# Optimization experiments

Hardware: AMD Instinct MI355X
Metric: run time of the kernel (lower is better)

## Reference

```python
import jax, jax.numpy as jnp
import numpy as np

ALPHA_MGD = 2e-05
NOISE_SIGMA = 8.0
NOISE_VAR = NOISE_SIGMA ** 2  # 64.0


def _conv2d(x, w, b, pad):
    # x: [N,C,H,W], w: [O,I,kh,kw]
    y = jax.lax.conv_general_dilated(
        x, w, window_strides=(1, 1), padding=[(pad, pad), (pad, pad)],
        dimension_numbers=("NCHW", "OIHW", "NCHW"))
    return y + b[None, :, None, None]


def setup_inputs() -> dict:
    key = jax.random.key(0)
    ks = jax.random.split(key, 8)
    N, Cs, Ct, H, W = 8, 128, 256, 64, 64
    return {
        "preds_S": jax.random.normal(ks[0], (N, Cs, H, W), jnp.float32),
        "preds_T": jax.random.normal(ks[1], (N, Ct, H, W), jnp.float32),
        "W_align": jax.random.normal(ks[2], (Ct, Cs, 1, 1), jnp.float32) * 0.05,
        "b_align": jnp.zeros((Ct,), jnp.float32),
        "W_gen1": jax.random.normal(ks[3], (Ct, Ct, 3, 3), jnp.float32) * 0.02,
        "b_gen1": jnp.zeros((Ct,), jnp.float32),
        "W_gen2": jax.random.normal(ks[4], (Ct, Ct, 3, 3), jnp.float32) * 0.02,
        "b_gen2": jnp.zeros((Ct,), jnp.float32),
    }


def reference(preds_S, preds_T, W_align, b_align, W_gen1, b_gen1, W_gen2, b_gen2):
    # align student channels to teacher channels (1x1 conv)
    s = _conv2d(preds_S, W_align, b_align, pad=0)
    N, C, H, W = preds_T.shape
    # deterministic checkerboard mask: tile([[0,1],[1,0]]) cropped to HxW -> (h+w) % 2
    hh = jnp.arange(H)[:, None]
    ww = jnp.arange(W)[None, :]
    mat = ((hh + ww) % 2).astype(s.dtype)  # [H,W]
    masked_fea = s * mat  # broadcast over [N,C,H,W]
    # generation network: conv3x3 -> relu -> conv3x3
    new_fea = _conv2d(jax.nn.relu(_conv2d(masked_fea, W_gen1, b_gen1, pad=1)), W_gen2, b_gen2, pad=1)
    # bmc_loss_md(pred=preds_T, target=new_fea, noise_var=64):
    # logits[i,j] = MVN(pred_i, noise_var*I).log_prob(target_j); the normalization
    # constant is class-independent and cancels in cross-entropy, keep the quadratic term.
    p = preds_T.reshape(N, -1)   # [N, D], D = C*H*W
    t = new_fea.reshape(N, -1)   # [N, D]
    # pairwise squared L2 via ||p||^2 + ||t||^2 - 2 p.t  (avoids NxNxD blow-up)
    sq = (jnp.sum(p * p, axis=1)[:, None]
          + jnp.sum(t * t, axis=1)[None, :]
          - 2.0 * (p @ t.T))  # [N, N]
    logits = -0.5 * sq / NOISE_VAR
    # cross_entropy(logits, arange(N)) = mean_i (logsumexp_j logits[i,j] - logits[i,i])
    ce = jnp.mean(jax.nn.logsumexp(logits, axis=1) - jnp.diagonal(logits))
    loss = ce * (2.0 * NOISE_VAR) / N
    return loss * ALPHA_MGD
```

## Files before the change

kernel.cpp:

```cpp
#include <hip/hip_runtime.h>

typedef unsigned short u16;
typedef short short8 __attribute__((ext_vector_type(8)));
typedef unsigned short ushort8 __attribute__((ext_vector_type(8)));
typedef float floatx16 __attribute__((ext_vector_type(16)));

#define PLANE8C  17952
#define NSTRIDEC 574464
#define PLANE8   34848
#define NSTRIDE  1115136

__device__ __forceinline__ u16 f2b(float f) {
  unsigned u = __builtin_bit_cast(unsigned, f);
  return (u16)((u + 0x7FFFu + ((u >> 16) & 1u)) >> 16);
}
__device__ __forceinline__ float b2f(u16 b) {
  return __builtin_bit_cast(float, ((unsigned)b) << 16);
}

typedef const __attribute__((address_space(1))) unsigned int* gptr_t;
typedef __attribute__((address_space(3))) unsigned int* sptr_t;

__global__ __launch_bounds__(256) void kprep(
    const float* __restrict__ Wg1, u16* __restrict__ Wsw1,
    const float* __restrict__ Wg2, u16* __restrict__ Wsw2,
    const float* __restrict__ Wa,  u16* __restrict__ Wb,
    const float* __restrict__ pS,  u16* __restrict__ T,
    u16* __restrict__ maskedC, u16* __restrict__ t1)
{
  __shared__ u16 Ls[64 * 136];
  int b = blockIdx.x, t = threadIdx.x;

  if (b < 576) {
    const float* W = (b < 288) ? Wg1 : Wg2;
    u16* D = (b < 288) ? Wsw1 : Wsw2;
    int bb = (b < 288) ? b : b - 288;
    int cid = bb * 256 + t;
    int d = cid % 1152, ctcg = cid / 1152;
    int ct = ctcg & 3, cg = ctcg >> 2;
    int colow = d & 31, cihalf = (d >> 5) & 1, sc = (d >> 6) & 1, tap = d >> 7;
    int co = ct * 64 + sc * 32 + colow;
    short8 v;
    #pragma unroll
    for (int jj = 0; jj < 8; ++jj) {
      int ci = cg * 16 + cihalf * 8 + jj;
      v[jj] = (short)f2b(W[((size_t)(co * 256 + ci)) * 9 + tap]);
    }
    *(short8*)&D[(size_t)cid * 8] = v;
  } else if (b < 592) {
    int v = (b - 576) * 256 + t;
    int colow = v & 31, hfb = (v >> 5) & 1, cog = (v >> 6) & 7, k = v >> 9;
    int co = cog * 32 + colow;
    int ci0 = k * 16 + hfb * 8;
    float4 f0 = *(const float4*)(Wa + (size_t)co * 128 + ci0);
    float4 f1 = *(const float4*)(Wa + (size_t)co * 128 + ci0 + 4);
    short8 o;
    o[0] = (short)f2b(f0.x); o[1] = (short)f2b(f0.y);
    o[2] = (short)f2b(f0.z); o[3] = (short)f2b(f0.w);
    o[4] = (short)f2b(f1.x); o[5] = (short)f2b(f1.y);
    o[6] = (short)f2b(f1.z); o[7] = (short)f2b(f1.w);
    *(short8*)&Wb[(size_t)v * 8] = o;
  } else if (b < 1104) {
    int bb = b - 592;
    int n = bb >> 6, pt = bb & 63, pix0 = pt * 64;
    int ci = t >> 1, ph = t & 1;
    const float* src = pS + ((size_t)n * 128 + ci) * 4096 + pix0 + ph * 32;
    #pragma unroll
    for (int i = 0; i < 8; ++i) {
      float4 v4 = *(const float4*)(src + i * 4);
      int pix = ph * 32 + i * 4;
      Ls[(pix + 0) * 136 + ci] = f2b(v4.x);
      Ls[(pix + 1) * 136 + ci] = f2b(v4.y);
      Ls[(pix + 2) * 136 + ci] = f2b(v4.z);
      Ls[(pix + 3) * 136 + ci] = f2b(v4.w);
    }
    __syncthreads();
    int p = t >> 2, q = t & 3;
    const u16* row = Ls + p * 136 + q * 32;
    u16* dst = T + ((size_t)n * 4096 + pix0 + p) * 128 + q * 32;
    #pragma unroll
    for (int k2 = 0; k2 < 4; ++k2)
      *(ushort8*)(dst + k2 * 8) = *(const ushort8*)(row + k2 * 8);
  } else if (b < 1360) {
    int p = b - 1104;
    u16* base = maskedC + (size_t)(p >> 5) * NSTRIDEC + (size_t)(p & 31) * PLANE8C;
    short8 z;
    #pragma unroll
    for (int jj = 0; jj < 8; ++jj) z[jj] = 0;
    if (t < 200) {
      int off;
      if (t < 34)       off = t * 8;
      else if (t < 68)  off = (65 * 34 + (t - 34)) * 8;
      else if (t < 134) off = ((t - 68) * 34) * 8;
      else              off = ((t - 134) * 34 + 33) * 8;
      *(short8*)(base + off) = z;
    }
  } else {
    int p = b - 1360;
    u16* base = t1 + (size_t)(p >> 5) * NSTRIDE + (size_t)(p & 31) * PLANE8;
    short8 z;
    #pragma unroll
    for (int jj = 0; jj < 8; ++jj) z[jj] = 0;
    #pragma unroll
    for (int pass = 0; pass < 2; ++pass) {
      int seg = t + pass * 256;
      if (seg < 264) {
        int off;
        if (seg < 66)       off = seg * 8;
        else if (seg < 132) off = (65 * 66 + (seg - 66)) * 8;
        else if (seg < 198) off = ((seg - 132) * 66) * 8;
        else                off = ((seg - 198) * 66 + 65) * 8;
        *(short8*)(base + off) = z;
      }
    }
  }
}

__global__ __launch_bounds__(256) void k1m(const u16* __restrict__ T,
    const u16* __restrict__ Wb, const float* __restrict__ ba,
    u16* __restrict__ mk)
{
  __shared__ __align__(16) u16 Wl[32768];
  int b = blockIdx.x;
  int n = b >> 5, pt = b & 31;
  int t = threadIdx.x, wid = t >> 6, lane = t & 63;
  int ml = lane & 31, hf = lane >> 5;

  #pragma unroll
  for (int kk = 0; kk < 16; ++kk) {
    int chunk = kk * 256 + t;
    __builtin_amdgcn_global_load_lds((gptr_t)(const void*)(Wb + (size_t)chunk * 8),
                                     (sptr_t)(void*)(Wl + chunk * 8), 16, 0, 0);
  }

  const u16* Tn = T + (size_t)n * 524288;
  const u16* ap[4];
  #pragma unroll
  for (int g = 0; g < 4; ++g)
    ap[g] = Tn + (size_t)(pt * 128 + g * 32 + ml) * 128 + hf * 8;

  floatx16 acc[2][4];
  #pragma unroll
  for (int q = 0; q < 2; ++q)
    #pragma unroll
    for (int g = 0; g < 4; ++g)
      #pragma unroll
      for (int i = 0; i < 16; ++i) acc[q][g][i] = 0.f;

  __syncthreads();

  const short8* WlV = (const short8*)Wl;
  int cogb = wid * 2;

  short8 a0[4], a1[4];
  #pragma unroll
  for (int g = 0; g < 4; ++g) a0[g] = *(const short8*)(ap[g]);

#define K1M_STEP(K, CUR, NXT, LAST)                                           \
  {                                                                           \
    if (!(LAST)) {                                                            \
      _Pragma("unroll")                                                       \
      for (int g = 0; g < 4; ++g)                                             \
        NXT[g] = *(const short8*)(ap[g] + ((K) + 1) * 16);                    \
    }                                                                         \
    short8 w0 = WlV[((K) * 8 + cogb) * 64 + lane];                            \
    short8 w1 = WlV[((K) * 8 + cogb + 1) * 64 + lane];                        \
    _Pragma("unroll")                                                         \
    for (int g = 0; g < 4; ++g) {                                             \
      acc[0][g] = __builtin_amdgcn_mfma_f32_32x32x16_bf16(CUR[g], w0, acc[0][g], 0, 0, 0); \
      acc[1][g] = __builtin_amdgcn_mfma_f32_32x32x16_bf16(CUR[g], w1, acc[1][g], 0, 0, 0); \
    }                                                                         \
  }
  K1M_STEP(0, a0, a1, 0)
  K1M_STEP(1, a1, a0, 0)
  K1M_STEP(2, a0, a1, 0)
  K1M_STEP(3, a1, a0, 0)
  K1M_STEP(4, a0, a1, 0)
  K1M_STEP(5, a1, a0, 0)
  K1M_STEP(6, a0, a1, 0)
  K1M_STEP(7, a1, a0, 1)
#undef K1M_STEP

  int co0 = cogb * 32 + ml, co1 = co0 + 32;
  float b0 = ba[co0], b1 = ba[co1];
  u16* base0 = mk + (size_t)n * NSTRIDEC + (size_t)(co0 >> 3) * PLANE8C + (co0 & 7);
  u16* base1 = mk + (size_t)n * NSTRIDEC + (size_t)(co1 >> 3) * PLANE8C + (co1 & 7);
  #pragma unroll
  for (int g = 0; g < 4; ++g)
    #pragma unroll
    for (int reg = 0; reg < 16; ++reg) {
      int m = (reg & 3) + 8 * (reg >> 2) + 4 * hf;
      int pix = pt * 128 + g * 32 + m;
      int h = pix >> 6, w = pix & 63;
      if (((h + w) & 1) == 1) {
        int j = (w - ((h + 1) & 1)) >> 1;
        int off = ((h + 1) * 34 + 1 + j) * 8;
        base0[off] = f2b(acc[0][g][reg] + b0);
        base1[off] = f2b(acc[1][g][reg] + b1);
      }
    }
}

__global__ __launch_bounds__(512) void kconvs(
    const u16* __restrict__ IN, const u16* __restrict__ WS,
    const float* __restrict__ bg, u16* __restrict__ OUT)
{
  __shared__ __align__(16) u16 L[30720];
  u16* LinA = L;
  u16* LwA  = L + 6144;
  u16* LinB = L + 15360;
  u16* LwB  = L + 21504;

  int b = blockIdx.x;
  int rt = b & 7, ct = (b >> 3) & 3, n = b >> 5;
  int h0 = rt * 8;
  int t = threadIdx.x;
  int wid = t >> 6, lane = t & 63;
  int hf = lane >> 5, ml = lane & 31;
  int e = wid & 1;

  const u16* inb = IN + (size_t)n * NSTRIDEC;
  const u16* wg  = WS + (size_t)ct * 1152 * 8;

  floatx16 acc[2][2];
  #pragma unroll
  for (int p = 0; p < 2; ++p)
    #pragma unroll
    for (int q = 0; q < 2; ++q)
      #pragma unroll
      for (int i = 0; i < 16; ++i) acc[p][q][i] = 0.f;

  auto STAGE = [&](int cg, u16* LinD, u16* LwD) {
    #pragma unroll
    for (int k = 0; k < 4; ++k) {
      int seg = wid + 8 * k;
      if (seg < 18) {
        const u16* src = wg + (size_t)cg * 36864 + (size_t)(seg * 64 + lane) * 8;
        __builtin_amdgcn_global_load_lds((gptr_t)(const void*)src,
                                         (sptr_t)(void*)(LwD + seg * 512), 16, 0, 0);
      } else if (seg < 30) {
        int ii = seg - 18;
        int hh = ii >= 6 ? 1 : 0;
        int s = ii - hh * 6;
        const u16* src = inb + (size_t)cg * (2 * PLANE8C) + (size_t)hh * PLANE8C
                         + (size_t)(h0 * 34 + s * 64 + lane) * 8;
        __builtin_amdgcn_global_load_lds((gptr_t)(const void*)src,
                                         (sptr_t)(void*)(LinD + (hh * 384 + s * 64) * 8),
                                         16, 0, 0);
      }
    }
  };

  auto COMPUTE = [&](const u16* LinS, const u16* LwS) {
    const short8* LinV = (const short8*)LinS;
    const short8* LwV  = (const short8*)LwS;
    int rA = hf * 384 + wid * 34 + 1 + ml;
    int rS = rA + 34;
    int rB = rA + 68;
    short8 iA0 = LinV[rA];
    short8 iS0 = LinV[rS];
    short8 iB0 = LinV[rB];
    short8 iSm = LinV[rS + e - 1];
    short8 iSp = LinV[rS + e];
    short8 iAm = LinV[rA - e];
    short8 iAp = LinV[rA + 1 - e];
    short8 iBm = LinV[rB - e];
    short8 iBp = LinV[rB + 1 - e];
    #pragma unroll
    for (int q = 0; q < 2; ++q) {
      short8 w0 = LwV[0 * 128 + q * 64 + lane];
      short8 w1 = LwV[1 * 128 + q * 64 + lane];
      short8 w2 = LwV[2 * 128 + q * 64 + lane];
      short8 w3 = LwV[3 * 128 + q * 64 + lane];
      short8 w4 = LwV[4 * 128 + q * 64 + lane];
      short8 w5 = LwV[5 * 128 + q * 64 + lane];
      short8 w6 = LwV[6 * 128 + q * 64 + lane];
      short8 w7 = LwV[7 * 128 + q * 64 + lane];
      short8 w8 = LwV[8 * 128 + q * 64 + lane];
      acc[0][q] = __builtin_amdgcn_mfma_f32_32x32x16_bf16(iA0, w1, acc[0][q], 0, 0, 0);
      acc[0][q] = __builtin_amdgcn_mfma_f32_32x32x16_bf16(iSm, w3, acc[0][q], 0, 0, 0);
      acc[0][q] = __builtin_amdgcn_mfma_f32_32x32x16_bf16(iSp, w5, acc[0][q], 0, 0, 0);
      acc[0][q] = __builtin_amdgcn_mfma_f32_32x32x16_bf16(iB0, w7, acc[0][q], 0, 0, 0);
      acc[1][q] = __builtin_amdgcn_mfma_f32_32x32x16_bf16(iAm, w0, acc[1][q], 0, 0, 0);
      acc[1][q] = __builtin_amdgcn_mfma_f32_32x32x16_bf16(iAp, w2, acc[1][q], 0, 0, 0);
      acc[1][q] = __builtin_amdgcn_mfma_f32_32x32x16_bf16(iS0, w4, acc[1][q], 0, 0, 0);
      acc[1][q] = __builtin_amdgcn_mfma_f32_32x32x16_bf16(iBm, w6, acc[1][q], 0, 0, 0);
      acc[1][q] = __builtin_amdgcn_mfma_f32_32x32x16_bf16(iBp, w8, acc[1][q], 0, 0, 0);
    }
  };

  STAGE(0, LinA, LwA);
  __syncthreads();
  for (int cg = 0; cg < 16; cg += 2) {
    STAGE(cg + 1, LinB, LwB);
    COMPUTE(LinA, LwA);
    __syncthreads();
    if (cg + 2 < 16) STAGE(cg + 2, LinA, LwA);
    COMPUTE(LinB, LwB);
    __syncthreads();
  }

  float bias0 = bg[ct * 64 + ml];
  float bias1 = bg[ct * 64 + 32 + ml];

  u16* ob = OUT + (size_t)n * NSTRIDE;
  int co0 = ct * 64 + ml, co1 = co0 + 32;
  int cb0 = ((co0 >> 4) * 2 + ((co0 >> 3) & 1)) * PLANE8 + (co0 & 7);
  int cb1 = ((co1 >> 4) * 2 + ((co1 >> 3) & 1)) * PLANE8 + (co1 & 7);
  int rowoff = (h0 + wid + 1) * 66 + 1;
  #pragma unroll
  for (int reg = 0; reg < 16; ++reg) {
    int m = (reg & 3) + 8 * (reg >> 2) + 4 * hf;
    int we = 2 * m + e, wo = 2 * m + 1 - e;
    float v;
    v = acc[0][0][reg] + bias0; v = fmaxf(v, 0.f); ob[cb0 + (rowoff + we) * 8] = f2b(v);
    v = acc[0][1][reg] + bias1; v = fmaxf(v, 0.f); ob[cb1 + (rowoff + we) * 8] = f2b(v);
    v = acc[1][0][reg] + bias0; v = fmaxf(v, 0.f); ob[cb0 + (rowoff + wo) * 8] = f2b(v);
    v = acc[1][1][reg] + bias1; v = fmaxf(v, 0.f); ob[cb1 + (rowoff + wo) * 8] = f2b(v);
  }
}

template <int MODE>
__global__ __launch_bounds__(512) void kconv(
    const u16* __restrict__ IN, const u16* __restrict__ WS,
    const float* __restrict__ bg, u16* __restrict__ OUT)
{
  __shared__ __align__(16) u16 L[40960];
  u16* LinA = L;
  u16* LwA  = L + 11264;
  u16* LinB = L + 20480;
  u16* LwB  = L + 31744;

  int b = blockIdx.x;
  int rt = b & 7, ct = (b >> 3) & 3, n = b >> 5;
  int h0 = rt * 8;
  int t = threadIdx.x;
  int wid = t >> 6, lane = t & 63;
  int hf = lane >> 5, ml = lane & 31;

  const u16* inb = IN + (size_t)n * NSTRIDE;
  const u16* wg  = WS + (size_t)ct * 1152 * 8;

  floatx16 acc[2][2];
  #pragma unroll
  for (int s = 0; s < 2; ++s)
    #pragma unroll
    for (int q = 0; q < 2; ++q)
      #pragma unroll
      for (int i = 0; i < 16; ++i) acc[s][q][i] = 0.f;

  auto STAGE = [&](int cg, u16* LinD, u16* LwD) {
    #pragma unroll
    for (int k = 0; k < 3; ++k) {
      int sidx = 8 * k + wid;
      if (sidx < 18) {
        const u16* src = wg + (size_t)cg * 36864 + (size_t)(sidx * 64 + lane) * 8;
        __builtin_amdgcn_global_load_lds((gptr_t)(const void*)src,
                                         (sptr_t)(void*)(LwD + sidx * 512), 16, 0, 0);
      }
    }
    #pragma unroll
    for (int k = 0; k < 3; ++k) {
      int seg = 8 * k + wid;
      if (seg < 22) {
        int half = seg >= 11 ? 1 : 0;
        int s = seg - half * 11;
        const u16* src = inb + (size_t)cg * 69696 + half * PLANE8
                         + (size_t)(h0 * 66 + s * 64 + lane) * 8;
        __builtin_amdgcn_global_load_lds((gptr_t)(const void*)src,
                                         (sptr_t)(void*)(LinD + (half * 704 + s * 64) * 8),
                                         16, 0, 0);
      }
    }
  };

  auto COMPUTE = [&](const u16* LinS, const u16* LwS) {
    const short8* LinV = (const short8*)LinS;
    const short8* LwV  = (const short8*)LwS;
    #pragma unroll
    for (int dr = 0; dr < 3; ++dr) {
      int r0 = hf * 704 + (wid + dr) * 66;
      #pragma unroll
      for (int dc = 0; dc < 3; ++dc) {
        int tap = dr * 3 + dc;
        short8 w0 = LwV[tap * 128 + lane];
        short8 w1 = LwV[tap * 128 + 64 + lane];
        short8 i0 = LinV[r0 + ml + dc];
        short8 i1 = LinV[r0 + 32 + ml + dc];
        acc[0][0] = __builtin_amdgcn_mfma_f32_32x32x16_bf16(i0, w0, acc[0][0], 0, 0, 0);
        acc[0][1] = __builtin_amdgcn_mfma_f32_32x32x16_bf16(i0, w1, acc[0][1], 0, 0, 0);
        acc[1][0] = __builtin_amdgcn_mfma_f32_32x32x16_bf16(i1, w0, acc[1][0], 0, 0, 0);
        acc[1][1] = __builtin_amdgcn_mfma_f32_32x32x16_bf16(i1, w1, acc[1][1], 0, 0, 0);
      }
    }
  };

  STAGE(0, LinA, LwA);
  __syncthreads();
  for (int cg = 0; cg < 16; cg += 2) {
    STAGE(cg + 1, LinB, LwB);
    COMPUTE(LinA, LwA);
    __syncthreads();
    if (cg + 2 < 16) STAGE(cg + 2, LinA, LwA);
    COMPUTE(LinB, LwB);
    __syncthreads();
  }

  float bias0 = bg[ct * 64 + ml];
  float bias1 = bg[ct * 64 + 32 + ml];

  if (MODE == 0) {
    u16* ob = OUT + (size_t)n * NSTRIDE;
    int co0 = ct * 64 + ml, co1 = co0 + 32;
    int cb0 = ((co0 >> 4) * 2 + ((co0 >> 3) & 1)) * PLANE8 + (co0 & 7);
    int cb1 = ((co1 >> 4) * 2 + ((co1 >> 3) & 1)) * PLANE8 + (co1 & 7);
    int rowoff = (h0 + wid + 1) * 66 + 1;
    #pragma unroll
    for (int reg = 0; reg < 16; ++reg) {
      int m = (reg & 3) + 8 * (reg >> 2) + 4 * hf;
      float v;
      v = acc[0][0][reg] + bias0; v = fmaxf(v, 0.f); ob[cb0 + (rowoff + m) * 8] = f2b(v);
      v = acc[0][1][reg] + bias1; v = fmaxf(v, 0.f); ob[cb1 + (rowoff + m) * 8] = f2b(v);
      v = acc[1][0][reg] + bias0; v = fmaxf(v, 0.f); ob[cb0 + (rowoff + 32 + m) * 8] = f2b(v);
      v = acc[1][1][reg] + bias1; v = fmaxf(v, 0.f); ob[cb1 + (rowoff + 32 + m) * 8] = f2b(v);
    }
  } else {
    u16* plane = L + wid * 4352;
    #pragma unroll
    for (int reg = 0; reg < 16; ++reg) {
      int m = (reg & 3) + 8 * (reg >> 2) + 4 * hf;
      plane[ml * 68 + m]              = f2b(acc[0][0][reg] + bias0);
      plane[(32 + ml) * 68 + m]       = f2b(acc[0][1][reg] + bias1);
      plane[ml * 68 + 32 + m]         = f2b(acc[1][0][reg] + bias0);
      plane[(32 + ml) * 68 + 32 + m]  = f2b(acc[1][1][reg] + bias1);
    }
    const u16* row = plane + lane * 68;
    __align__(16) u16 tmp[64];
    #pragma unroll
    for (int k2 = 0; k2 < 16; ++k2)
      *(ushort4*)(tmp + k2 * 4) = *(const ushort4*)(row + k2 * 4);
    u16* gdst = OUT + (size_t)n * 1048576 + (size_t)(ct * 64 + lane) * 4096
                + (h0 + wid) * 64;
    #pragma unroll
    for (int k2 = 0; k2 < 8; ++k2)
      *(ushort8*)(gdst + k2 * 8) = *(const ushort8*)(tmp + k2 * 8);
  }
}

__global__ __launch_bounds__(256) void kbmc(const u16* __restrict__ t2,
    const float* __restrict__ pT, float* __restrict__ part)
{
  int t = threadIdx.x, lane = t & 63, role = t >> 6;
  int ih = role >> 1, nh = role & 1;
  int bid = blockIdx.x;

  float pt[4][4], pp[4], tt[4];
  #pragma unroll
  for (int i = 0; i < 4; ++i) {
    pp[i] = 0.f; tt[i] = 0.f;
    #pragma unroll
    for (int j = 0; j < 4; ++j) pt[i][j] = 0.f;
  }

  const float* pb = pT + ((size_t)ih * 4) * 1048576;
  const u16*   tb = t2 + ((size_t)nh * 4) * 1048576;

  for (int k = 0; k < 8; ++k) {
    size_t d0 = ((size_t)(bid * 512 + k * 64 + lane)) * 4;
    float4 p[4], tf[4];
    #pragma unroll
    for (int i = 0; i < 4; ++i)
      p[i] = *(const float4*)(pb + (size_t)i * 1048576 + d0);
    #pragma unroll
    for (int j = 0; j < 4; ++j) {
      ushort4 tv = *(const ushort4*)(tb + (size_t)j * 1048576 + d0);
      tf[j] = make_float4(b2f(tv.x), b2f(tv.y), b2f(tv.z), b2f(tv.w));
    }
    if (nh == 0) {
      #pragma unroll
      for (int i = 0; i < 4; ++i)
        pp[i] += p[i].x * p[i].x + p[i].y * p[i].y + p[i].z * p[i].z + p[i].w * p[i].w;
    }
    if (ih == 0) {
      #pragma unroll
      for (int j = 0; j < 4; ++j)
        tt[j] += tf[j].x * tf[j].x + tf[j].y * tf[j].y + tf[j].z * tf[j].z + tf[j].w * tf[j].w;
    }
    #pragma unroll
    for (int i = 0; i < 4; ++i)
      #pragma unroll
      for (int j = 0; j < 4; ++j)
        pt[i][j] += p[i].x * tf[j].x + p[i].y * tf[j].y
                  + p[i].z * tf[j].z + p[i].w * tf[j].w;
  }

  #pragma unroll
  for (int m = 1; m < 64; m <<= 1) {
    #pragma unroll
    for (int i = 0; i < 4; ++i) {
      pp[i] += __shfl_xor(pp[i], m);
      tt[i] += __shfl_xor(tt[i], m);
      #pragma unroll
      for (int j = 0; j < 4; ++j) pt[i][j] += __shfl_xor(pt[i][j], m);
    }
  }
  if (lane == 0) {
    #pragma unroll
    for (int i = 0; i < 4; ++i)
      #pragma unroll
      for (int j = 0; j < 4; ++j)
        part[(size_t)(16 + (ih * 4 + i) * 8 + (nh * 4 + j)) * 512 + bid] = pt[i][j];
    if (nh == 0) {
      #pragma unroll
      for (int i = 0; i < 4; ++i) part[(size_t)(ih * 4 + i) * 512 + bid] = pp[i];
    }
    if (ih == 0) {
      #pragma unroll
      for (int j = 0; j < 4; ++j) part[(size_t)(8 + nh * 4 + j) * 512 + bid] = tt[j];
    }
  }
}

__global__ __launch_bounds__(256) void kred(const float* __restrict__ part,
                                            float* __restrict__ accums)
{
  __shared__ float r4[4];
  int s = blockIdx.x, t = threadIdx.x, lane = t & 63, wid = t >> 6;
  float v = part[(size_t)s * 512 + t] + part[(size_t)s * 512 + 256 + t];
  #pragma unroll
  for (int m = 1; m < 64; m <<= 1) v += __shfl_xor(v, m);
  if (lane == 0) r4[wid] = v;
  __syncthreads();
  if (t == 0) accums[s] = r4[0] + r4[1] + r4[2] + r4[3];
}

__global__ void k4_final(const float* __restrict__ accums, float* __restrict__ out)
{
  int t = threadIdx.x;
  int i = t >> 3, j = t & 7;
  double pp = accums[i];
  double tt = accums[8 + j];
  double pt = accums[16 + i * 8 + j];
  double logit = -0.5 * (pp + tt - 2.0 * pt) / 64.0;
  double m = logit;
  #pragma unroll
  for (int s = 1; s < 8; s <<= 1) {
    double o = __shfl_xor(m, s);
    m = o > m ? o : m;
  }
  double e = exp(logit - m);
  #pragma unroll
  for (int s = 1; s < 8; s <<= 1) e += __shfl_xor(e, s);
  double lse = m + log(e);
  double term = (j == i) ? (lse - logit) : 0.0;
  #pragma unroll
  for (int s = 1; s < 64; s <<= 1) term += __shfl_xor(term, s);
  if (t == 0) {
    double ce = term / 8.0;
    out[0] = (float)(ce * (2.0 * 64.0) / 8.0 * 2e-05);
  }
}

extern "C" void kernel_launch(void* const* d_in, const int* in_sizes, int n_in,
                              void* d_out, int out_size, void* d_ws, size_t ws_size,
                              hipStream_t stream)
{
  const float* preds_S = (const float*)d_in[0];
  const float* preds_T = (const float*)d_in[1];
  const float* W_align = (const float*)d_in[2];
  const float* b_align = (const float*)d_in[3];
  const float* W_gen1  = (const float*)d_in[4];
  const float* b_gen1  = (const float*)d_in[5];
  const float* W_gen2  = (const float*)d_in[6];
  const float* b_gen2  = (const float*)d_in[7];
  float* out = (float*)d_out;

  char* wsb = (char*)d_ws;
  u16* maskedC = (u16*)wsb;
  u16* t1     = (u16*)(wsb + 9191424);
  u16* t2p    = (u16*)(wsb + 27033600);
  u16* T      = t2p;
  u16* Wsw1   = (u16*)(wsb + 43810816);
  u16* Wsw2   = (u16*)(wsb + 44990464);
  float* part   = (float*)(wsb + 46170112);
  float* accums = (float*)(wsb + 46366720);
  u16* Wb     = (u16*)(wsb + 46367104);

  kprep<<<1616, 256, 0, stream>>>(W_gen1, Wsw1, W_gen2, Wsw2, W_align, Wb,
                                  preds_S, T, maskedC, t1);
  k1m<<<256, 256, 0, stream>>>(T, Wb, b_align, maskedC);
  kconvs<<<256, 512, 0, stream>>>(maskedC, Wsw1, b_gen1, t1);
  kconv<1><<<256, 512, 0, stream>>>(t1, Wsw2, b_gen2, t2p);
  kbmc<<<512, 256, 0, stream>>>(t2p, preds_T, part);
  kred<<<80, 256, 0, stream>>>(part, accums);
  k4_final<<<1, 64, 0, stream>>>(accums, out);
}
```

Measured before the change: 192.7 us.

## Stage two channel groups per barrier in conv1 and fuse final reduction kernels

The first 3x3 conv kernel now stages two channel groups per double-buffer slot, using 120 KB of LDS instead of 60 KB. This halves the number of __syncthreads barriers and issues larger batches of async global-to-LDS loads. The final reduction and loss kernels are merged using an atomic counter, which kprep zeroes, so the last block computes the loss and one kernel launch is dropped. The risks are that the larger LDS footprint may limit occupancy and that the atomic/last-block pattern adds fences.

```diff
diff --git a/kernel.cpp b/kernel.cpp
--- a/kernel.cpp
+++ b/kernel.cpp
@@ -26,7 +26,8 @@
     const float* __restrict__ Wg2, u16* __restrict__ Wsw2,
     const float* __restrict__ Wa,  u16* __restrict__ Wb,
     const float* __restrict__ pS,  u16* __restrict__ T,
-    u16* __restrict__ maskedC, u16* __restrict__ t1)
+    u16* __restrict__ maskedC, u16* __restrict__ t1,
+    unsigned int* __restrict__ cnt)
 {
   __shared__ u16 Ls[64 * 136];
   int b = blockIdx.x, t = threadIdx.x;
@@ -95,7 +96,7 @@
       else              off = ((t - 134) * 34 + 33) * 8;
       *(short8*)(base + off) = z;
     }
-  } else {
+  } else if (b < 1616) {
     int p = b - 1360;
     u16* base = t1 + (size_t)(p >> 5) * NSTRIDE + (size_t)(p & 31) * PLANE8;
     short8 z;
@@ -113,6 +114,8 @@
         *(short8*)(base + off) = z;
       }
     }
+  } else {
+    if (t == 0) *cnt = 0u;
   }
 }
 
@@ -205,11 +208,9 @@
     const u16* __restrict__ IN, const u16* __restrict__ WS,
     const float* __restrict__ bg, u16* __restrict__ OUT)
 {
-  __shared__ __align__(16) u16 L[30720];
-  u16* LinA = L;
-  u16* LwA  = L + 6144;
-  u16* LinB = L + 15360;
-  u16* LwB  = L + 21504;
+  __shared__ __align__(16) u16 L[61440];
+  u16* LA = L;
+  u16* LB = L + 30720;
 
   int b = blockIdx.x;
   int rt = b & 7, ct = (b >> 3) & 3, n = b >> 5;
@@ -230,73 +231,84 @@
       #pragma unroll
       for (int i = 0; i < 16; ++i) acc[p][q][i] = 0.f;
 
-  auto STAGE = [&](int cg, u16* LinD, u16* LwD) {
-    #pragma unroll
-    for (int k = 0; k < 4; ++k) {
+  auto STAGE2 = [&](int cgp, u16* B) {
+    u16* inD = B;
+    u16* LwD = B + 12288;
+    #pragma unroll
+    for (int k = 0; k < 8; ++k) {
       int seg = wid + 8 * k;
-      if (seg < 18) {
-        const u16* src = wg + (size_t)cg * 36864 + (size_t)(seg * 64 + lane) * 8;
-        __builtin_amdgcn_global_load_lds((gptr_t)(const void*)src,
-                                         (sptr_t)(void*)(LwD + seg * 512), 16, 0, 0);
-      } else if (seg < 30) {
-        int ii = seg - 18;
-        int hh = ii >= 6 ? 1 : 0;
-        int s = ii - hh * 6;
-        const u16* src = inb + (size_t)cg * (2 * PLANE8C) + (size_t)hh * PLANE8C
-                         + (size_t)(h0 * 34 + s * 64 + lane) * 8;
-        __builtin_amdgcn_global_load_lds((gptr_t)(const void*)src,
-                                         (sptr_t)(void*)(LinD + (hh * 384 + s * 64) * 8),
-                                         16, 0, 0);
+      if (seg < 60) {
+        int c = seg >= 30 ? 1 : 0;
+        int ss = seg - c * 30;
+        int cg = cgp * 2 + c;
+        if (ss < 18) {
+          const u16* src = wg + (size_t)cg * 36864 + (size_t)(ss * 64 + lane) * 8;
+          __builtin_amdgcn_global_load_lds((gptr_t)(const void*)src,
+                                           (sptr_t)(void*)(LwD + c * 9216 + ss * 512),
+                                           16, 0, 0);
+        } else {
+          int ii = ss - 18;
+          int hh = ii >= 6 ? 1 : 0;
+          int s = ii - hh * 6;
+          const u16* src = inb + (size_t)cg * (2 * PLANE8C) + (size_t)hh * PLANE8C
+                           + (size_t)(h0 * 34 + s * 64 + lane) * 8;
+          __builtin_amdgcn_global_load_lds((gptr_t)(const void*)src,
+                                           (sptr_t)(void*)(inD + c * 6144 + (hh * 384 + s * 64) * 8),
+                                           16, 0, 0);
+        }
       }
     }
   };
 
-  auto COMPUTE = [&](const u16* LinS, const u16* LwS) {
-    const short8* LinV = (const short8*)LinS;
-    const short8* LwV  = (const short8*)LwS;
-    int rA = hf * 384 + wid * 34 + 1 + ml;
-    int rS = rA + 34;
-    int rB = rA + 68;
-    short8 iA0 = LinV[rA];
-    short8 iS0 = LinV[rS];
-    short8 iB0 = LinV[rB];
-    short8 iSm = LinV[rS + e - 1];
-    short8 iSp = LinV[rS + e];
-    short8 iAm = LinV[rA - e];
-    short8 iAp = LinV[rA + 1 - e];
-    short8 iBm = LinV[rB - e];
-    short8 iBp = LinV[rB + 1 - e];
-    #pragma unroll
-    for (int q = 0; q < 2; ++q) {
-      short8 w0 = LwV[0 * 128 + q * 64 + lane];
-      short8 w1 = LwV[1 * 128 + q * 64 + lane];
-      short8 w2 = LwV[2 * 128 + q * 64 + lane];
-      short8 w3 = LwV[3 * 128 + q * 64 + lane];
-      short8 w4 = LwV[4 * 128 + q * 64 + lane];
-      short8 w5 = LwV[5 * 128 + q * 64 + lane];
-      short8 w6 = LwV[6 * 128 + q * 64 + lane];
-      short8 w7 = LwV[7 * 128 + q * 64 + lane];
-      short8 w8 = LwV[8 * 128 + q * 64 + lane];
-      acc[0][q] = __builtin_amdgcn_mfma_f32_32x32x16_bf16(iA0, w1, acc[0][q], 0, 0, 0);
-      acc[0][q] = __builtin_amdgcn_mfma_f32_32x32x16_bf16(iSm, w3, acc[0][q], 0, 0, 0);
-      acc[0][q] = __builtin_amdgcn_mfma_f32_32x32x16_bf16(iSp, w5, acc[0][q], 0, 0, 0);
-      acc[0][q] = __builtin_amdgcn_mfma_f32_32x32x16_bf16(iB0, w7, acc[0][q], 0, 0, 0);
-      acc[1][q] = __builtin_amdgcn_mfma_f32_32x32x16_bf16(iAm, w0, acc[1][q], 0, 0, 0);
-      acc[1][q] = __builtin_amdgcn_mfma_f32_32x32x16_bf16(iAp, w2, acc[1][q], 0, 0, 0);
-      acc[1][q] = __builtin_amdgcn_mfma_f32_32x32x16_bf16(iS0, w4, acc[1][q], 0, 0, 0);
-      acc[1][q] = __builtin_amdgcn_mfma_f32_32x32x16_bf16(iBm, w6, acc[1][q], 0, 0, 0);
-      acc[1][q] = __builtin_amdgcn_mfma_f32_32x32x16_bf16(iBp, w8, acc[1][q], 0, 0, 0);
+  auto COMPUTE2 = [&](const u16* B) {
+    #pragma unroll
+    for (int c = 0; c < 2; ++c) {
+      const short8* LinV = (const short8*)B + c * 768;
+      const short8* LwV  = (const short8*)B + 1536 + c * 1152;
+      int rA = hf * 384 + wid * 34 + 1 + ml;
+      int rS = rA + 34;
+      int rB = rA + 68;
+      short8 iA0 = LinV[rA];
+      short8 iS0 = LinV[rS];
+      short8 iB0 = LinV[rB];
+      short8 iSm = LinV[rS + e - 1];
+      short8 iSp = LinV[rS + e];
+      short8 iAm = LinV[rA - e];
+      short8 iAp = LinV[rA + 1 - e];
+      short8 iBm = LinV[rB - e];
+      short8 iBp = LinV[rB + 1 - e];
+      #pragma unroll
+      for (int q = 0; q < 2; ++q) {
+        short8 w0 = LwV[0 * 128 + q * 64 + lane];
+        short8 w1 = LwV[1 * 128 + q * 64 + lane];
+        short8 w2 = LwV[2 * 128 + q * 64 + lane];
+        short8 w3 = LwV[3 * 128 + q * 64 + lane];
+        short8 w4 = LwV[4 * 128 + q * 64 + lane];
+        short8 w5 = LwV[5 * 128 + q * 64 + lane];
+        short8 w6 = LwV[6 * 128 + q * 64 + lane];
+        short8 w7 = LwV[7 * 128 + q * 64 + lane];
+        short8 w8 = LwV[8 * 128 + q * 64 + lane];
+        acc[0][q] = __builtin_amdgcn_mfma_f32_32x32x16_bf16(iA0, w1, acc[0][q], 0, 0, 0);
+        acc[0][q] = __builtin_amdgcn_mfma_f32_32x32x16_bf16(iSm, w3, acc[0][q], 0, 0, 0);
+        acc[0][q] = __builtin_amdgcn_mfma_f32_32x32x16_bf16(iSp, w5, acc[0][q], 0, 0, 0);
+        acc[0][q] = __builtin_amdgcn_mfma_f32_32x32x16_bf16(iB0, w7, acc[0][q], 0, 0, 0);
+        acc[1][q] = __builtin_amdgcn_mfma_f32_32x32x16_bf16(iAm, w0, acc[1][q], 0, 0, 0);
+        acc[1][q] = __builtin_amdgcn_mfma_f32_32x32x16_bf16(iAp, w2, acc[1][q], 0, 0, 0);
+        acc[1][q] = __builtin_amdgcn_mfma_f32_32x32x16_bf16(iS0, w4, acc[1][q], 0, 0, 0);
+        acc[1][q] = __builtin_amdgcn_mfma_f32_32x32x16_bf16(iBm, w6, acc[1][q], 0, 0, 0);
+        acc[1][q] = __builtin_amdgcn_mfma_f32_32x32x16_bf16(iBp, w8, acc[1][q], 0, 0, 0);
+      }
     }
   };
 
-  STAGE(0, LinA, LwA);
+  STAGE2(0, LA);
   __syncthreads();
-  for (int cg = 0; cg < 16; cg += 2) {
-    STAGE(cg + 1, LinB, LwB);
-    COMPUTE(LinA, LwA);
+  for (int p = 0; p < 8; p += 2) {
+    STAGE2(p + 1, LB);
+    COMPUTE2(LA);
     __syncthreads();
-    if (cg + 2 < 16) STAGE(cg + 2, LinA, LwA);
-    COMPUTE(LinB, LwB);
+    if (p + 2 < 8) STAGE2(p + 2, LA);
+    COMPUTE2(LB);
     __syncthreads();
   }
 
@@ -521,43 +533,49 @@
   }
 }
 
-__global__ __launch_bounds__(256) void kred(const float* __restrict__ part,
-                                            float* __restrict__ accums)
+__global__ __launch_bounds__(256) void kred2(const float* __restrict__ part,
+    float* __restrict__ accums, unsigned int* __restrict__ cnt,
+    float* __restrict__ out)
 {
   __shared__ float r4[4];
+  __shared__ int last;
   int s = blockIdx.x, t = threadIdx.x, lane = t & 63, wid = t >> 6;
   float v = part[(size_t)s * 512 + t] + part[(size_t)s * 512 + 256 + t];
   #pragma unroll
   for (int m = 1; m < 64; m <<= 1) v += __shfl_xor(v, m);
   if (lane == 0) r4[wid] = v;
   __syncthreads();
-  if (t == 0) accums[s] = r4[0] + r4[1] + r4[2] + r4[3];
-}
-
-__global__ void k4_final(const float* __restrict__ accums, float* __restrict__ out)
-{
-  int t = threadIdx.x;
-  int i = t >> 3, j = t & 7;
-  double pp = accums[i];
-  double tt = accums[8 + j];
-  double pt = accums[16 + i * 8 + j];
-  double logit = -0.5 * (pp + tt - 2.0 * pt) / 64.0;
-  double m = logit;
-  #pragma unroll
-  for (int s = 1; s < 8; s <<= 1) {
-    double o = __shfl_xor(m, s);
-    m = o > m ? o : m;
-  }
-  double e = exp(logit - m);
-  #pragma unroll
-  for (int s = 1; s < 8; s <<= 1) e += __shfl_xor(e, s);
-  double lse = m + log(e);
-  double term = (j == i) ? (lse - logit) : 0.0;
-  #pragma unroll
-  for (int s = 1; s < 64; s <<= 1) term += __shfl_xor(term, s);
   if (t == 0) {
-    double ce = term / 8.0;
-    out[0] = (float)(ce * (2.0 * 64.0) / 8.0 * 2e-05);
+    atomicExch(&accums[s], r4[0] + r4[1] + r4[2] + r4[3]);
+    __threadfence();
+    unsigned int old = atomicAdd(cnt, 1u);
+    last = (old == 79u) ? 1 : 0;
+  }
+  __syncthreads();
+  if (last && t < 64) {
+    __threadfence();
+    int i = t >> 3, j = t & 7;
+    double pp = (double)atomicAdd(&accums[i], 0.0f);
+    double tt = (double)atomicAdd(&accums[8 + j], 0.0f);
+    double pt = (double)atomicAdd(&accums[16 + i * 8 + j], 0.0f);
+    double logit = -0.5 * (pp + tt - 2.0 * pt) / 64.0;
+    double m = logit;
+    #pragma unroll
+    for (int ss = 1; ss < 8; ss <<= 1) {
+      double o = __shfl_xor(m, ss);
+      m = o > m ? o : m;
+    }
+    double e = exp(logit - m);
+    #pragma unroll
+    for (int ss = 1; ss < 8; ss <<= 1) e += __shfl_xor(e, ss);
+    double lse = m + log(e);
+    double term = (j == i) ? (lse - logit) : 0.0;
+    #pragma unroll
+    for (int ss = 1; ss < 64; ss <<= 1) term += __shfl_xor(term, ss);
+    if (t == 0) {
+      double ce = term / 8.0;
+      out[0] = (float)(ce * (2.0 * 64.0) / 8.0 * 2e-05);
+    }
   }
 }
 
@@ -585,13 +603,13 @@
   float* part   = (float*)(wsb + 46170112);
   float* accums = (float*)(wsb + 46366720);
   u16* Wb     = (u16*)(wsb + 46367104);
-
-  kprep<<<1616, 256, 0, stream>>>(W_gen1, Wsw1, W_gen2, Wsw2, W_align, Wb,
-                                  preds_S, T, maskedC, t1);
+  unsigned int* cnt = (unsigned int*)(wsb + 46432640);
+
+  kprep<<<1617, 256, 0, stream>>>(W_gen1, Wsw1, W_gen2, Wsw2, W_align, Wb,
+                                  preds_S, T, maskedC, t1, cnt);
   k1m<<<256, 256, 0, stream>>>(T, Wb, b_align, maskedC);
   kconvs<<<256, 512, 0, stream>>>(maskedC, Wsw1, b_gen1, t1);
   kconv<1><<<256, 512, 0, stream>>>(t1, Wsw2, b_gen2, t2p);
   kbmc<<<512, 256, 0, stream>>>(t2p, preds_T, part);
-  kred<<<80, 256, 0, stream>>>(part, accums);
-  k4_final<<<1, 64, 0, stream>>>(accums, out);
-}
+  kred2<<<80, 256, 0, stream>>>(part, accums, cnt, out);
+}
```

Result: slower. 197.0 us (+2.2%).
